# Optimization experiments

Measured on AMD Instinct MI355X. Metric: run time of the kernel, lower is better.

## Reference

```python
import jax, jax.numpy as jnp
import numpy as np

NUM_LAYERS = 3
HIDDEN = 64
NUM_CLASSES = 4096
LN_EPS = 1e-5


def setup_inputs() -> dict:
    key = jax.random.key(0)
    ks = jax.random.split(key, 8)
    B, N, E, H = 8, NUM_CLASSES, 131072, HIDDEN
    node_features = jax.random.normal(ks[0], (B, N, H), dtype=jnp.float32)
    edge_indices = jax.random.randint(ks[1], (B, 2, E), 0, N, dtype=jnp.int64)
    edge_attrs = jax.random.normal(ks[2], (B, E, H), dtype=jnp.float32)
    # GraphConvolutionLayer params (xavier_uniform weight, zero bias) per layer
    limit = np.sqrt(6.0 / (H + H)).astype(np.float32)
    W = jax.random.uniform(ks[3], (NUM_LAYERS, H, H), minval=-limit, maxval=limit, dtype=jnp.float32)
    b = jnp.zeros((NUM_LAYERS, H), dtype=jnp.float32)
    gamma = jnp.ones((NUM_LAYERS, H), dtype=jnp.float32)
    beta = jnp.zeros((NUM_LAYERS, H), dtype=jnp.float32)
    global_emb = 0.02 * jax.random.normal(ks[4], (N, H), dtype=jnp.float32)
    return {
        "node_features": node_features,
        "edge_indices": edge_indices,
        "edge_attrs": edge_attrs,
        "W": W,
        "b": b,
        "gamma": gamma,
        "beta": beta,
        "global_emb": global_emb,
    }


def _layer_norm(x, g, bt):
    mu = jnp.mean(x, axis=-1, keepdims=True)
    var = jnp.mean((x - mu) ** 2, axis=-1, keepdims=True)
    return (x - mu) * jax.lax.rsqrt(var + LN_EPS) * g + bt


def reference(node_features, edge_indices, edge_attrs, W, b, gamma, beta, global_emb):
    N = node_features.shape[1]

    def per_graph(x0, ei, ea):
        # presence mask computed on raw node features [N, 1]
        presence = (jnp.sum(x0, axis=1) != 0).astype(x0.dtype)[:, None]
        src, dst = ei[0], ei[1]
        x = x0
        for i in range(NUM_LAYERS):
            residual = x
            h = x @ W[i]                                   # [N, H]
            msg = h[src] * ea                              # gather + edge gate [E, H]
            out = jax.ops.segment_sum(msg, dst, num_segments=N) + b[i]
            out = jax.nn.relu(out)
            out = _layer_norm(out, gamma[i], beta[i])
            x = out + residual if i > 0 else out
        return x * presence + global_emb * (1.0 - presence)

    return jax.vmap(per_graph)(node_features, edge_indices, edge_attrs)
```

## Files before the change

### kernel.cpp

```cpp
#include <hip/hip_runtime.h>

#define GB 8
#define GN 4096
#define GH 64
#define GE 131072
#define LN_EPS 1e-5f
#define NBIN (GB * GN)
#define TOTE (GB * GE)

__global__ void k_init(const float* __restrict__ nf, float* __restrict__ pres) {
    int w = (blockIdx.x * blockDim.x + threadIdx.x) >> 6;
    int lane = threadIdx.x & 63;
    if (w >= NBIN) return;
    float v = nf[(size_t)w * GH + lane];
    #pragma unroll
    for (int o = 1; o < 64; o <<= 1) v += __shfl_xor(v, o, 64);
    if (lane == 0) pres[w] = (v != 0.0f) ? 1.0f : 0.0f;
}

__global__ void k_hist(const int* __restrict__ ei, int* __restrict__ hist) {
    int t = blockIdx.x * blockDim.x + threadIdx.x;
    int b = t >> 17, e = t & (GE - 1);
    int dst = ei[(b << 18) + GE + e];
    atomicAdd(&hist[(b << 12) + dst], 1);
}

__global__ void k_scan(const int* __restrict__ hist, int* __restrict__ off,
                       int* __restrict__ cur) {
    __shared__ int part[256];
    int b = blockIdx.x;
    int t = threadIdx.x;
    int base = (b << 12) + t * 16;
    int c[16];
    int s = 0;
    #pragma unroll
    for (int i = 0; i < 16; ++i) { c[i] = hist[base + i]; s += c[i]; }
    part[t] = s;
    __syncthreads();
    for (int o = 1; o < 256; o <<= 1) {
        int u = (t >= o) ? part[t - o] : 0;
        __syncthreads();
        part[t] += u;
        __syncthreads();
    }
    int p = b * GE + part[t] - s;
    #pragma unroll
    for (int i = 0; i < 16; ++i) { off[base + i] = p; cur[base + i] = p; p += c[i]; }
    if (b == GB - 1 && t == 255) off[NBIN] = TOTE;
}

__global__ void k_fill(const int* __restrict__ ei, int* __restrict__ cur,
                       int2* __restrict__ sPair) {
    int t = blockIdx.x * blockDim.x + threadIdx.x;
    int b = t >> 17, e = t & (GE - 1);
    int src = ei[(b << 18) + e];
    int dst = ei[(b << 18) + GE + e];
    int pos = atomicAdd(&cur[(b << 12) + dst], 1);
    sPair[pos] = make_int2(src, t);
}

__global__ void k_gemm(const float* __restrict__ x, const float* __restrict__ W,
                       float* __restrict__ h, int layer) {
    __shared__ float Wl[GH * GH];
    for (int i = threadIdx.x; i < GH * GH; i += blockDim.x)
        Wl[i] = W[layer * GH * GH + i];
    __syncthreads();
    int w = (blockIdx.x * blockDim.x + threadIdx.x) >> 6;
    int lane = threadIdx.x & 63;
    if (w >= NBIN) return;
    float xv = x[(size_t)w * GH + lane];
    float acc = 0.0f;
    #pragma unroll
    for (int k = 0; k < GH; ++k)
        acc = fmaf(__shfl(xv, k, 64), Wl[k * GH + lane], acc);
    h[(size_t)w * GH + lane] = acc;
}

__global__ void k_gather(const int* __restrict__ off, const int2* __restrict__ sPair,
                         const float* __restrict__ ea, const float* __restrict__ h,
                         const float* __restrict__ bias, const float* __restrict__ gam,
                         const float* __restrict__ bet,
                         float* __restrict__ x, const float* __restrict__ pres,
                         const float* __restrict__ ge, float* __restrict__ out,
                         int layer) {
    int w = (blockIdx.x * blockDim.x + threadIdx.x) >> 6;
    int lane = threadIdx.x & 63;
    if (w >= NBIN) return;
    int b = w >> 12;
    int beg = off[w], end = off[w + 1];
    int cnt = end - beg;
    const float* hb = h + (((size_t)b) << 12) * GH;
    int fg = (lane & 15) << 2;
    int g  = lane >> 4;

    float4 acc = make_float4(0.f, 0.f, 0.f, 0.f);
    for (int base = 0; base < cnt; base += 64) {
        int n = min(cnt - base, 64);
        int2 pr = make_int2(0, 0);
        if (lane < n) pr = sPair[beg + base + lane];
        for (int j = 0; j < n; j += 8) {
            int j0 = j + g, j1 = j + 4 + g;
            int s0 = __shfl(pr.x, j0), r0 = __shfl(pr.y, j0);
            int s1 = __shfl(pr.x, j1), r1 = __shfl(pr.y, j1);
            if (j0 < n) {
                float4 ev = *reinterpret_cast<const float4*>(ea + ((size_t)r0 << 6) + fg);
                float4 hv = *reinterpret_cast<const float4*>(hb + ((size_t)s0 << 6) + fg);
                acc.x = fmaf(ev.x, hv.x, acc.x);
                acc.y = fmaf(ev.y, hv.y, acc.y);
                acc.z = fmaf(ev.z, hv.z, acc.z);
                acc.w = fmaf(ev.w, hv.w, acc.w);
            }
            if (j1 < n) {
                float4 ev = *reinterpret_cast<const float4*>(ea + ((size_t)r1 << 6) + fg);
                float4 hv = *reinterpret_cast<const float4*>(hb + ((size_t)s1 << 6) + fg);
                acc.x = fmaf(ev.x, hv.x, acc.x);
                acc.y = fmaf(ev.y, hv.y, acc.y);
                acc.z = fmaf(ev.z, hv.z, acc.z);
                acc.w = fmaf(ev.w, hv.w, acc.w);
            }
        }
    }
    #pragma unroll
    for (int o = 16; o < 64; o <<= 1) {
        acc.x += __shfl_xor(acc.x, o, 64);
        acc.y += __shfl_xor(acc.y, o, 64);
        acc.z += __shfl_xor(acc.z, o, 64);
        acc.w += __shfl_xor(acc.w, o, 64);
    }
    int srcl = lane >> 2;
    float c0 = __shfl(acc.x, srcl);
    float c1 = __shfl(acc.y, srcl);
    float c2 = __shfl(acc.z, srcl);
    float c3 = __shfl(acc.w, srcl);
    int cc = lane & 3;
    float v = (cc == 0) ? c0 : (cc == 1) ? c1 : (cc == 2) ? c2 : c3;

    v = fmaxf(v + bias[layer * GH + lane], 0.0f);
    float s = v;
    #pragma unroll
    for (int o = 1; o < 64; o <<= 1) s += __shfl_xor(s, o, 64);
    float mu = s * (1.0f / GH);
    float d = v - mu;
    float q = d * d;
    #pragma unroll
    for (int o = 1; o < 64; o <<= 1) q += __shfl_xor(q, o, 64);
    float var = q * (1.0f / GH);
    float y = d * rsqrtf(var + LN_EPS) * gam[layer * GH + lane] + bet[layer * GH + lane];
    size_t idx = (size_t)w * GH + lane;
    if (layer > 0) y += x[idx];
    if (layer < 2) {
        x[idx] = y;
    } else {
        float p = pres[w];
        float g2 = ge[(size_t)(w & (GN - 1)) * GH + lane];
        out[idx] = y * p + g2 * (1.0f - p);
    }
}

extern "C" void kernel_launch(void* const* d_in, const int* in_sizes, int n_in,
                              void* d_out, int out_size, void* d_ws, size_t ws_size,
                              hipStream_t stream) {
    const float* nf = (const float*)d_in[0];
    const int* ei   = (const int*)d_in[1];
    const float* ea = (const float*)d_in[2];
    const float* W  = (const float*)d_in[3];
    const float* bb = (const float*)d_in[4];
    const float* gg = (const float*)d_in[5];
    const float* be = (const float*)d_in[6];
    const float* ge = (const float*)d_in[7];
    float* out = (float*)d_out;

    float* x    = (float*)d_ws;
    float* h    = x + (size_t)NBIN * GH;
    float* pres = h + (size_t)NBIN * GH;
    int* off    = (int*)(pres + NBIN);
    int* cur    = off + NBIN + 1;
    int* hist   = cur + NBIN;
    int2* sPair = (int2*)(hist + NBIN);

    hipMemsetAsync(hist, 0, NBIN * sizeof(int), stream);
    k_init<<<NBIN / 4, 256, 0, stream>>>(nf, pres);
    k_hist<<<TOTE / 256, 256, 0, stream>>>(ei, hist);
    k_scan<<<GB, 256, 0, stream>>>(hist, off, cur);
    k_fill<<<TOTE / 256, 256, 0, stream>>>(ei, cur, sPair);

    for (int l = 0; l < 3; ++l) {
        k_gemm<<<NBIN / 4, 256, 0, stream>>>(l == 0 ? nf : x, W, h, l);
        k_gather<<<NBIN / 4, 256, 0, stream>>>(off, sPair, ea, h, bb, gg, be,
                                               x, pres, ge, out, l);
    }
}
```

Before: 423.4 us.

## Permute edge attributes into CSR order as bf16 and store h in bf16

```diff
diff --git a/kernel.cpp b/kernel.cpp
--- a/kernel.cpp
+++ b/kernel.cpp
@@ -7,6 +7,15 @@
 #define LN_EPS 1e-5f
 #define NBIN (GB * GN)
 #define TOTE (GB * GE)
+
+static __device__ __forceinline__ float bfu(unsigned short u) {
+    union { float f; unsigned int i; } v; v.i = ((unsigned int)u) << 16; return v.f;
+}
+static __device__ __forceinline__ unsigned short f2bf(float f) {
+    union { float f; unsigned int u; } v; v.f = f;
+    unsigned int u = v.u;
+    return (unsigned short)((u + 0x7FFFu + ((u >> 16) & 1u)) >> 16);
+}
 
 __global__ void k_init(const float* __restrict__ nf, float* __restrict__ pres) {
     int w = (blockIdx.x * blockDim.x + threadIdx.x) >> 6;
@@ -49,18 +58,27 @@
     if (b == GB - 1 && t == 255) off[NBIN] = TOTE;
 }
 
-__global__ void k_fill(const int* __restrict__ ei, int* __restrict__ cur,
-                       int2* __restrict__ sPair) {
-    int t = blockIdx.x * blockDim.x + threadIdx.x;
-    int b = t >> 17, e = t & (GE - 1);
-    int src = ei[(b << 18) + e];
+__global__ void k_fillperm(const int* __restrict__ ei, int* __restrict__ cur,
+                           const float* __restrict__ ea,
+                           int* __restrict__ sSrc, unsigned short* __restrict__ ea_s) {
+    int grp = (blockIdx.x * blockDim.x + threadIdx.x) >> 4;
+    if (grp >= TOTE) return;
+    int sub  = threadIdx.x & 15;
+    int lane = threadIdx.x & 63;
+    int b = grp >> 17, e = grp & (GE - 1);
     int dst = ei[(b << 18) + GE + e];
-    int pos = atomicAdd(&cur[(b << 12) + dst], 1);
-    sPair[pos] = make_int2(src, t);
+    int pos = 0;
+    if (sub == 0) pos = atomicAdd(&cur[(b << 12) + dst], 1);
+    pos = __shfl(pos, lane & ~15, 64);
+    float4 v = *reinterpret_cast<const float4*>(ea + ((size_t)grp << 6) + (sub << 2));
+    ushort4 o;
+    o.x = f2bf(v.x); o.y = f2bf(v.y); o.z = f2bf(v.z); o.w = f2bf(v.w);
+    *reinterpret_cast<ushort4*>(ea_s + ((size_t)pos << 6) + (sub << 2)) = o;
+    if (sub == 0) sSrc[pos] = ei[(b << 18) + e];
 }
 
 __global__ void k_gemm(const float* __restrict__ x, const float* __restrict__ W,
-                       float* __restrict__ h, int layer) {
+                       unsigned short* __restrict__ h, int layer) {
     __shared__ float Wl[GH * GH];
     for (int i = threadIdx.x; i < GH * GH; i += blockDim.x)
         Wl[i] = W[layer * GH * GH + i];
@@ -73,11 +91,12 @@
     #pragma unroll
     for (int k = 0; k < GH; ++k)
         acc = fmaf(__shfl(xv, k, 64), Wl[k * GH + lane], acc);
-    h[(size_t)w * GH + lane] = acc;
-}
-
-__global__ void k_gather(const int* __restrict__ off, const int2* __restrict__ sPair,
-                         const float* __restrict__ ea, const float* __restrict__ h,
+    h[(size_t)w * GH + lane] = f2bf(acc);
+}
+
+__global__ void k_gather(const int* __restrict__ off, const int* __restrict__ sSrc,
+                         const unsigned short* __restrict__ ea_s,
+                         const unsigned short* __restrict__ h,
                          const float* __restrict__ bias, const float* __restrict__ gam,
                          const float* __restrict__ bet,
                          float* __restrict__ x, const float* __restrict__ pres,
@@ -89,34 +108,33 @@
     int b = w >> 12;
     int beg = off[w], end = off[w + 1];
     int cnt = end - beg;
-    const float* hb = h + (((size_t)b) << 12) * GH;
+    const unsigned short* hb = h + (((size_t)b) << 12) * GH;
     int fg = (lane & 15) << 2;
     int g  = lane >> 4;
 
     float4 acc = make_float4(0.f, 0.f, 0.f, 0.f);
     for (int base = 0; base < cnt; base += 64) {
         int n = min(cnt - base, 64);
-        int2 pr = make_int2(0, 0);
-        if (lane < n) pr = sPair[beg + base + lane];
+        int sv = (lane < n) ? sSrc[beg + base + lane] : 0;
         for (int j = 0; j < n; j += 8) {
             int j0 = j + g, j1 = j + 4 + g;
-            int s0 = __shfl(pr.x, j0), r0 = __shfl(pr.y, j0);
-            int s1 = __shfl(pr.x, j1), r1 = __shfl(pr.y, j1);
+            int s0 = __shfl(sv, j0);
+            int s1 = __shfl(sv, j1);
             if (j0 < n) {
-                float4 ev = *reinterpret_cast<const float4*>(ea + ((size_t)r0 << 6) + fg);
-                float4 hv = *reinterpret_cast<const float4*>(hb + ((size_t)s0 << 6) + fg);
-                acc.x = fmaf(ev.x, hv.x, acc.x);
-                acc.y = fmaf(ev.y, hv.y, acc.y);
-                acc.z = fmaf(ev.z, hv.z, acc.z);
-                acc.w = fmaf(ev.w, hv.w, acc.w);
+                ushort4 ev = *reinterpret_cast<const ushort4*>(ea_s + ((size_t)(beg + base + j0) << 6) + fg);
+                ushort4 hv = *reinterpret_cast<const ushort4*>(hb + ((size_t)s0 << 6) + fg);
+                acc.x = fmaf(bfu(ev.x), bfu(hv.x), acc.x);
+                acc.y = fmaf(bfu(ev.y), bfu(hv.y), acc.y);
+                acc.z = fmaf(bfu(ev.z), bfu(hv.z), acc.z);
+                acc.w = fmaf(bfu(ev.w), bfu(hv.w), acc.w);
             }
             if (j1 < n) {
-                float4 ev = *reinterpret_cast<const float4*>(ea + ((size_t)r1 << 6) + fg);
-                float4 hv = *reinterpret_cast<const float4*>(hb + ((size_t)s1 << 6) + fg);
-                acc.x = fmaf(ev.x, hv.x, acc.x);
-                acc.y = fmaf(ev.y, hv.y, acc.y);
-                acc.z = fmaf(ev.z, hv.z, acc.z);
-                acc.w = fmaf(ev.w, hv.w, acc.w);
+                ushort4 ev = *reinterpret_cast<const ushort4*>(ea_s + ((size_t)(beg + base + j1) << 6) + fg);
+                ushort4 hv = *reinterpret_cast<const ushort4*>(hb + ((size_t)s1 << 6) + fg);
+                acc.x = fmaf(bfu(ev.x), bfu(hv.x), acc.x);
+                acc.y = fmaf(bfu(ev.y), bfu(hv.y), acc.y);
+                acc.z = fmaf(bfu(ev.z), bfu(hv.z), acc.z);
+                acc.w = fmaf(bfu(ev.w), bfu(hv.w), acc.w);
             }
         }
     }
@@ -171,22 +189,23 @@
     float* out = (float*)d_out;
 
     float* x    = (float*)d_ws;
-    float* h    = x + (size_t)NBIN * GH;
-    float* pres = h + (size_t)NBIN * GH;
+    float* pres = x + (size_t)NBIN * GH;
     int* off    = (int*)(pres + NBIN);
     int* cur    = off + NBIN + 1;
     int* hist   = cur + NBIN;
-    int2* sPair = (int2*)(hist + NBIN);
+    int* sSrc   = hist + NBIN;
+    unsigned short* h_s  = (unsigned short*)(sSrc + TOTE);
+    unsigned short* ea_s = h_s + (size_t)NBIN * GH;
 
     hipMemsetAsync(hist, 0, NBIN * sizeof(int), stream);
     k_init<<<NBIN / 4, 256, 0, stream>>>(nf, pres);
     k_hist<<<TOTE / 256, 256, 0, stream>>>(ei, hist);
     k_scan<<<GB, 256, 0, stream>>>(hist, off, cur);
-    k_fill<<<TOTE / 256, 256, 0, stream>>>(ei, cur, sPair);
+    k_fillperm<<<TOTE / 16, 256, 0, stream>>>(ei, cur, ea, sSrc, ea_s);
 
     for (int l = 0; l < 3; ++l) {
-        k_gemm<<<NBIN / 4, 256, 0, stream>>>(l == 0 ? nf : x, W, h, l);
-        k_gather<<<NBIN / 4, 256, 0, stream>>>(off, sPair, ea, h, bb, gg, be,
+        k_gemm<<<NBIN / 4, 256, 0, stream>>>(l == 0 ? nf : x, W, h_s, l);
+        k_gather<<<NBIN / 4, 256, 0, stream>>>(off, sSrc, ea_s, h_s, bb, gg, be,
                                                x, pres, ge, out, l);
     }
 }
```

After: 426.8 us. About the same (+0.8%).
